# Performance work log

Measured on AMD Instinct MI355X. Metric: run time of the kernel, lower is better.

The kernel has to match this reference:

```python
import jax, jax.numpy as jnp
import numpy as np

C = 512        # feat_dim
T_LEN = 8192   # sequence length
N = 16384      # number of proposals
HID = 1024     # hidden_dim
OUT = 512      # out_dim
RATIO = 0.15   # boundary_ratio


def setup_inputs() -> dict:
    key = jax.random.key(0)
    ks = jax.random.split(key, 6)
    feat_map = jax.random.normal(ks[0], (C, T_LEN), jnp.float32)
    l = jax.random.randint(ks[1], (N,), 0, T_LEN - 64)
    width = jax.random.randint(ks[2], (N,), 8, 512)
    r = jnp.minimum(l + width, T_LEN - 1)
    W1 = jax.random.normal(ks[3], (HID, 2 * C), jnp.float32) * 0.02
    b1 = jnp.zeros((HID,), jnp.float32)
    W2 = jax.random.normal(ks[4], (OUT, HID), jnp.float32) * 0.02
    b2 = jnp.zeros((OUT,), jnp.float32)
    return {
        "feat_map": feat_map,
        "l": l.astype(jnp.int32),
        "r": r.astype(jnp.int32),
        "T": T_LEN,
        "W1": W1, "b1": b1, "W2": W2, "b2": b2,
    }


def _boundary_regions(l, r, T):
    # Mirrors: w = max(r-l, 1.0); bw = max(1, int(ratio*w)); clipped windows.
    lf = l.astype(jnp.float32)
    rf = r.astype(jnp.float32)
    w = jnp.maximum(rf - lf, 1.0)
    bw = jnp.maximum(1, (RATIO * w).astype(jnp.int32))  # int() truncation (w > 0)
    rl = jnp.round(lf).astype(jnp.int32)
    rr = jnp.round(rf).astype(jnp.int32)
    lb_s = jnp.maximum(0, rl - bw)
    lb_e = jnp.minimum(T, rl + bw)
    rb_s = jnp.maximum(0, rr - bw)
    rb_e = jnp.minimum(T, rr + bw)
    return lb_s, lb_e, rb_s, rb_e


def _pool(cs, s, e, T):
    # mean of feat[:, s:e] via inclusive prefix sums; cs: (C, T+1)
    e = jnp.maximum(s + 1, e)
    e = jnp.minimum(e, T)
    seg = cs[:, e] - cs[:, s]                      # (C, N)
    return (seg / (e - s).astype(cs.dtype)).T      # (N, C)


def reference(feat_map, l, r, T, W1, b1, W2, b2):
    # feat_map: (C, T); l, r: (N,) int proposal boundaries
    cs = jnp.concatenate(
        [jnp.zeros((feat_map.shape[0], 1), feat_map.dtype),
         jnp.cumsum(feat_map, axis=1)], axis=1)    # (C, T+1)
    lb_s, lb_e, rb_s, rb_e = _boundary_regions(l, r, T)
    e_left = _pool(cs, lb_s, lb_e, T)              # (N, C)
    e_right = _pool(cs, rb_s, rb_e, T)             # (N, C)
    e = jnp.concatenate([e_left, e_right], axis=-1)  # (N, 2C)
    h = jax.nn.relu(e @ W1.T + b1)                 # (N, HID)
    return h @ W2.T + b2                           # (N, OUT)
```

## Files before the change

### kernel.cpp

```cpp
#include <hip/hip_runtime.h>
#include <hip/hip_bf16.h>
#include <stdint.h>

#define C_DIM 512
#define T_SEQ 8192
#define N_PROP 16384
#define HID_DIM 1024
#define OUT_DIM 512
#define K2C 1024

typedef __attribute__((ext_vector_type(8))) __bf16 bf16x8;
typedef __attribute__((ext_vector_type(4))) float f32x4;

#define CFENCE() asm volatile("" ::: "memory")

__global__ __launch_bounds__(64) void cumsum_kernel(const float* __restrict__ feat,
                                                    float* __restrict__ cs_inc) {
    int c = blockIdx.x;
    const float4* in = (const float4*)(feat + (size_t)c * T_SEQ);
    float4* out = (float4*)(cs_inc + (size_t)c * T_SEQ);
    int lane = threadIdx.x;
    float carry = 0.0f;
    for (int i0 = 0; i0 < T_SEQ / 4; i0 += 64) {
        float4 v = in[i0 + lane];
        float s1 = v.x + v.y;
        float s2 = s1 + v.z;
        float s3 = s2 + v.w;
        float x = s3;
#pragma unroll
        for (int s = 1; s < 64; s <<= 1) {
            float y = __shfl_up(x, s);
            if (lane >= s) x += y;
        }
        float base = carry + (x - s3);
        float4 o;
        o.x = base + v.x; o.y = base + s1; o.z = base + s2; o.w = base + s3;
        out[i0 + lane] = o;
        carry += __shfl(x, 63);
    }
}

__global__ __launch_bounds__(256) void transpose_kernel(const float* __restrict__ cs_inc,
                                                        float* __restrict__ cs_t) {
    __shared__ float tl[32][33];
    int tx = threadIdx.x, ty = threadIdx.y;
    int x0 = blockIdx.x * 32;
    int y0 = blockIdx.y * 32;
#pragma unroll
    for (int i = 0; i < 32; i += 8) {
        int t = x0 + tx;
        int ch = y0 + ty + i;
        float v = 0.0f;
        if (t >= 1 && t <= T_SEQ) v = cs_inc[(size_t)ch * T_SEQ + (t - 1)];
        tl[ty + i][tx] = v;
    }
    __syncthreads();
#pragma unroll
    for (int i = 0; i < 32; i += 8) {
        int t = x0 + ty + i;
        int ch = y0 + tx;
        if (t <= T_SEQ) cs_t[(size_t)t * C_DIM + ch] = tl[tx][ty + i];
    }
}

__global__ __launch_bounds__(512) void pool_kernel(const float* __restrict__ cs_t,
                                                   const int* __restrict__ lptr,
                                                   const int* __restrict__ rptr,
                                                   __hip_bfloat16* __restrict__ e) {
    int n = blockIdx.x * 4 + (threadIdx.x >> 7);
    int c4 = (threadIdx.x & 127) * 4;
    int li = lptr[n], ri = rptr[n];
    float w = fmaxf((float)(ri - li), 1.0f);
    int bw = max(1, (int)(0.15f * w));
    int lb_s = max(0, li - bw);
    int lb_e = min(T_SEQ, li + bw);
    int rb_s = max(0, ri - bw);
    int rb_e = min(T_SEQ, ri + bw);
    lb_e = min(max(lb_s + 1, lb_e), T_SEQ);
    rb_e = min(max(rb_s + 1, rb_e), T_SEQ);
    float4 a = *(const float4*)(cs_t + (size_t)lb_e * C_DIM + c4);
    float4 b = *(const float4*)(cs_t + (size_t)lb_s * C_DIM + c4);
    float4 cc = *(const float4*)(cs_t + (size_t)rb_e * C_DIM + c4);
    float4 d = *(const float4*)(cs_t + (size_t)rb_s * C_DIM + c4);
    float rl = 1.0f / (float)(lb_e - lb_s);
    float rr = 1.0f / (float)(rb_e - rb_s);
    __hip_bfloat16 L0 = __float2bfloat16((a.x - b.x) * rl);
    __hip_bfloat16 L1 = __float2bfloat16((a.y - b.y) * rl);
    __hip_bfloat16 L2 = __float2bfloat16((a.z - b.z) * rl);
    __hip_bfloat16 L3 = __float2bfloat16((a.w - b.w) * rl);
    __hip_bfloat16 R0 = __float2bfloat16((cc.x - d.x) * rr);
    __hip_bfloat16 R1 = __float2bfloat16((cc.y - d.y) * rr);
    __hip_bfloat16 R2 = __float2bfloat16((cc.z - d.z) * rr);
    __hip_bfloat16 R3 = __float2bfloat16((cc.w - d.w) * rr);
    ushort4 ul, ur;
    ul.x = *(unsigned short*)&L0; ul.y = *(unsigned short*)&L1;
    ul.z = *(unsigned short*)&L2; ul.w = *(unsigned short*)&L3;
    ur.x = *(unsigned short*)&R0; ur.y = *(unsigned short*)&R1;
    ur.z = *(unsigned short*)&R2; ur.w = *(unsigned short*)&R3;
    *(ushort4*)(e + (size_t)n * K2C + c4) = ul;
    *(ushort4*)(e + (size_t)n * K2C + C_DIM + c4) = ur;
}

__global__ __launch_bounds__(256) void cvt_bf16_kernel(const float* __restrict__ W1,
                                                       const float* __restrict__ W2,
                                                       __hip_bfloat16* __restrict__ W1b,
                                                       __hip_bfloat16* __restrict__ W2b) {
    const int n1 = HID_DIM * K2C;
    int i = (blockIdx.x * 256 + threadIdx.x) * 4;
    const float* src;
    __hip_bfloat16* dst;
    int j;
    if (i < n1) { src = W1; dst = W1b; j = i; }
    else        { src = W2; dst = W2b; j = i - n1; }
    float4 v = *(const float4*)(src + j);
    __hip_bfloat16 h0 = __float2bfloat16(v.x);
    __hip_bfloat16 h1 = __float2bfloat16(v.y);
    __hip_bfloat16 h2 = __float2bfloat16(v.z);
    __hip_bfloat16 h3 = __float2bfloat16(v.w);
    ushort4 u;
    u.x = *(unsigned short*)&h0; u.y = *(unsigned short*)&h1;
    u.z = *(unsigned short*)&h2; u.w = *(unsigned short*)&h3;
    *(ushort4*)(dst + j) = u;
}

template <int BM, int BN, int WM, int WN, int RELU_BF16>
__global__ __launch_bounds__(512, 2) void gemm_pipe_kernel(const __hip_bfloat16* __restrict__ A,
                                                           const __hip_bfloat16* __restrict__ B,
                                                           const float* __restrict__ bias,
                                                           void* __restrict__ Cout,
                                                           int Nc, int K, int NBlk) {
    constexpr int BK = 64;
    constexpr int WMT = BM / WM;
    constexpr int WNT = BN / WN;
    constexpr int MR = WMT / 16;
    constexpr int NR = WNT / 16;
    constexpr int LA = BM / 64;
    constexpr int LB = BN / 64;

    __shared__ __align__(16) __hip_bfloat16 As[2][BM * BK];
    __shared__ __align__(16) __hip_bfloat16 Bs[2][BN * BK];

    const int tid = threadIdx.x;
    const int lane = tid & 63;
    const int wid = tid >> 6;
    const int wm = wid / WN;
    const int wn = wid % WN;

    const int nwg = gridDim.x;
    const int wg = (blockIdx.x & 7) * (nwg >> 3) + (blockIdx.x >> 3);
    const long m0 = (long)(wg / NBlk) * BM;
    const long n0 = (long)(wg % NBlk) * BN;

    const int srow = tid >> 3;
    const int schunk = (tid & 7) ^ (srow & 7);
    const int fr = lane & 15;
    const int g8 = (lane >> 4) * 8;

    f32x4 acc[MR][NR] = {};

    auto stageA = [&](int s, int k0) {
#pragma unroll
        for (int i = 0; i < LA; ++i)
            __builtin_amdgcn_global_load_lds(
                (const __attribute__((address_space(1))) void*)(A + (m0 + i * 64 + srow) * K + k0 + schunk * 8),
                (__attribute__((address_space(3))) void*)(&As[s][i * 4096 + tid * 8]), 16, 0, 0);
    };
    auto stageB = [&](int s, int k0) {
#pragma unroll
        for (int i = 0; i < LB; ++i)
            __builtin_amdgcn_global_load_lds(
                (const __attribute__((address_space(1))) void*)(B + (n0 + i * 64 + srow) * K + k0 + schunk * 8),
                (__attribute__((address_space(3))) void*)(&Bs[s][i * 4096 + tid * 8]), 16, 0, 0);
    };
    auto ldfrag = [&](const __hip_bfloat16* buf, int row, int kbase) -> bf16x8 {
        return *(const bf16x8*)(buf + row * 64 + ((kbase + g8) ^ ((row & 7) * 8)));
    };

    const int NT = K / BK;
    stageA(0, 0);
    stageB(0, 0);
    for (int t = 0; t < NT; ++t) {
        const int cur = t & 1;
        const __hip_bfloat16* Asc = &As[cur][0];
        const __hip_bfloat16* Bsc = &Bs[cur][0];
        if (t + 1 < NT) {
            stageA(cur ^ 1, (t + 1) * BK);
            asm volatile("s_waitcnt vmcnt(%0)" ::"n"(LA) : "memory");
        } else {
            asm volatile("s_waitcnt vmcnt(0)" ::: "memory");
        }
        __builtin_amdgcn_s_barrier();
        CFENCE();
        {
            bf16x8 af[MR], bv[NR];
#pragma unroll
            for (int m = 0; m < MR; ++m) af[m] = ldfrag(Asc, wm * WMT + m * 16 + fr, 0);
#pragma unroll
            for (int n = 0; n < NR; ++n) bv[n] = ldfrag(Bsc, wn * WNT + n * 16 + fr, 0);
            __builtin_amdgcn_s_setprio(1);
#pragma unroll
            for (int m = 0; m < MR; ++m)
#pragma unroll
                for (int n = 0; n < NR; ++n)
                    acc[m][n] = __builtin_amdgcn_mfma_f32_16x16x32_bf16(af[m], bv[n], acc[m][n], 0, 0, 0);
            __builtin_amdgcn_s_setprio(0);
        }
        if (t + 1 < NT) stageB(cur ^ 1, (t + 1) * BK);
        {
            bf16x8 af[MR], bv[NR];
#pragma unroll
            for (int m = 0; m < MR; ++m) af[m] = ldfrag(Asc, wm * WMT + m * 16 + fr, 32);
#pragma unroll
            for (int n = 0; n < NR; ++n) bv[n] = ldfrag(Bsc, wn * WNT + n * 16 + fr, 32);
            __builtin_amdgcn_s_setprio(1);
#pragma unroll
            for (int m = 0; m < MR; ++m)
#pragma unroll
                for (int n = 0; n < NR; ++n)
                    acc[m][n] = __builtin_amdgcn_mfma_f32_16x16x32_bf16(af[m], bv[n], acc[m][n], 0, 0, 0);
            __builtin_amdgcn_s_setprio(0);
        }
        CFENCE();
        __builtin_amdgcn_s_barrier();
    }

    const int rq = (lane >> 4) * 4;
#pragma unroll
    for (int m = 0; m < MR; ++m)
#pragma unroll
        for (int n = 0; n < NR; ++n) {
            long col = n0 + wn * WNT + n * 16 + fr;
            float bb = bias[col];
#pragma unroll
            for (int q = 0; q < 4; ++q) {
                long row = m0 + wm * WMT + m * 16 + rq + q;
                float v = acc[m][n][q] + bb;
                if (RELU_BF16) {
                    v = fmaxf(v, 0.0f);
                    ((__hip_bfloat16*)Cout)[row * Nc + col] = __float2bfloat16(v);
                } else {
                    ((float*)Cout)[row * Nc + col] = v;
                }
            }
        }
}

extern "C" void kernel_launch(void* const* d_in, const int* in_sizes, int n_in,
                              void* d_out, int out_size, void* d_ws, size_t ws_size,
                              hipStream_t stream) {
    const float* feat = (const float*)d_in[0];
    const int* l = (const int*)d_in[1];
    const int* r = (const int*)d_in[2];
    const float* W1 = (const float*)d_in[4];
    const float* b1 = (const float*)d_in[5];
    const float* W2 = (const float*)d_in[6];
    const float* b2 = (const float*)d_in[7];

    char* ws = (char*)d_ws;
    float* cs_t = (float*)ws;
    __hip_bfloat16* e = (__hip_bfloat16*)(ws + 16779264);
    __hip_bfloat16* h = (__hip_bfloat16*)(ws + 50333696);
    float* cs_inc = (float*)(ws + 50333696);
    __hip_bfloat16* W1b = (__hip_bfloat16*)(ws + 83888128);
    __hip_bfloat16* W2b = (__hip_bfloat16*)(ws + 85985280);

    const int ncvt = (HID_DIM * K2C + OUT_DIM * HID_DIM) / 4 / 256;
    cvt_bf16_kernel<<<dim3(ncvt), 256, 0, stream>>>(W1, W2, W1b, W2b);
    cumsum_kernel<<<dim3(C_DIM), 64, 0, stream>>>(feat, cs_inc);
    transpose_kernel<<<dim3((T_SEQ + 32) / 32, C_DIM / 32), dim3(32, 8), 0, stream>>>(cs_inc, cs_t);
    pool_kernel<<<dim3(N_PROP / 4), 512, 0, stream>>>(cs_t, l, r, e);

    gemm_pipe_kernel<256, 256, 2, 4, 1>
        <<<dim3((N_PROP / 256) * (HID_DIM / 256)), 512, 0, stream>>>(e, W1b, b1, h, HID_DIM, K2C, HID_DIM / 256);
    gemm_pipe_kernel<256, 128, 4, 2, 0>
        <<<dim3((N_PROP / 256) * (OUT_DIM / 128)), 512, 0, stream>>>(h, W2b, b2, d_out, OUT_DIM, HID_DIM, OUT_DIM / 128);
}
```

Measured before the change: 117.8 us.

## Restructure GEMM mainloop into fine-grained interleaved load/MFMA phases

Replaces the two-stage GEMM loop with a phased schedule that splits each K-tile's MFMA work into several barrier-delimited chunks. It spreads the global-to-LDS loads for the next (and next-next) tile across those chunks and prefetches part of tile u+2 into the current buffer. The goal is to hide memory latency and even out the issue of loads against matrix-core work across waves. The cost is many more barriers per iteration, and the hand-counted vmcnt waits must match the load counts exactly, which makes the schedule fragile.

New measurement: 113.1 us. 1.04x faster.

```diff
diff --git a/kernel.cpp b/kernel.cpp
--- a/kernel.cpp
+++ b/kernel.cpp
@@ -11,8 +11,6 @@
 
 typedef __attribute__((ext_vector_type(8))) __bf16 bf16x8;
 typedef __attribute__((ext_vector_type(4))) float f32x4;
-
-#define CFENCE() asm volatile("" ::: "memory")
 
 __global__ __launch_bounds__(64) void cumsum_kernel(const float* __restrict__ feat,
                                                     float* __restrict__ cs_inc) {
@@ -123,19 +121,18 @@
     *(ushort4*)(dst + j) = u;
 }
 
-template <int BM, int BN, int WM, int WN, int RELU_BF16>
-__global__ __launch_bounds__(512, 2) void gemm_pipe_kernel(const __hip_bfloat16* __restrict__ A,
-                                                           const __hip_bfloat16* __restrict__ B,
-                                                           const float* __restrict__ bias,
-                                                           void* __restrict__ Cout,
-                                                           int Nc, int K, int NBlk) {
+template <int BM, int BN, int WM, int WN, int MQ, int RELU_BF16>
+__global__ __launch_bounds__(512, 2) void gemm8p_kernel(const __hip_bfloat16* __restrict__ A,
+                                                        const __hip_bfloat16* __restrict__ B,
+                                                        const float* __restrict__ bias,
+                                                        void* __restrict__ Cout,
+                                                        int Nc, int K, int NBlk) {
     constexpr int BK = 64;
-    constexpr int WMT = BM / WM;
-    constexpr int WNT = BN / WN;
-    constexpr int MR = WMT / 16;
-    constexpr int NR = WNT / 16;
-    constexpr int LA = BM / 64;
-    constexpr int LB = BN / 64;
+    constexpr int WMT = BM / WM, WNT = BN / WN;
+    constexpr int MR = WMT / 16, NR = WNT / 16;
+    constexpr int LA = BM / 64, LB = BN / 64;
+    constexpr int U = LA + LB;
+    constexpr int CL = (MQ == 2) ? 2 : 3;
 
     __shared__ __align__(16) __hip_bfloat16 As[2][BM * BK];
     __shared__ __align__(16) __hip_bfloat16 Bs[2][BN * BK];
@@ -158,70 +155,131 @@
 
     f32x4 acc[MR][NR] = {};
 
-    auto stageA = [&](int s, int k0) {
-#pragma unroll
-        for (int i = 0; i < LA; ++i)
+    auto stage_one = [&](int s, int k0, int i) {
+        if (i < LA)
             __builtin_amdgcn_global_load_lds(
                 (const __attribute__((address_space(1))) void*)(A + (m0 + i * 64 + srow) * K + k0 + schunk * 8),
                 (__attribute__((address_space(3))) void*)(&As[s][i * 4096 + tid * 8]), 16, 0, 0);
+        else
+            __builtin_amdgcn_global_load_lds(
+                (const __attribute__((address_space(1))) void*)(B + (n0 + (i - LA) * 64 + srow) * K + k0 + schunk * 8),
+                (__attribute__((address_space(3))) void*)(&Bs[s][(i - LA) * 4096 + tid * 8]), 16, 0, 0);
     };
-    auto stageB = [&](int s, int k0) {
-#pragma unroll
-        for (int i = 0; i < LB; ++i)
-            __builtin_amdgcn_global_load_lds(
-                (const __attribute__((address_space(1))) void*)(B + (n0 + i * 64 + srow) * K + k0 + schunk * 8),
-                (__attribute__((address_space(3))) void*)(&Bs[s][i * 4096 + tid * 8]), 16, 0, 0);
+    auto ldfragA = [&](int s, int row, int kbase) -> bf16x8 {
+        return *(const bf16x8*)(&As[s][row * 64 + ((kbase + g8) ^ ((row & 7) * 8))]);
     };
-    auto ldfrag = [&](const __hip_bfloat16* buf, int row, int kbase) -> bf16x8 {
-        return *(const bf16x8*)(buf + row * 64 + ((kbase + g8) ^ ((row & 7) * 8)));
+    auto ldfragB = [&](int s, int row, int kbase) -> bf16x8 {
+        return *(const bf16x8*)(&Bs[s][row * 64 + ((kbase + g8) ^ ((row & 7) * 8))]);
     };
 
     const int NT = K / BK;
-    stageA(0, 0);
-    stageB(0, 0);
-    for (int t = 0; t < NT; ++t) {
-        const int cur = t & 1;
-        const __hip_bfloat16* Asc = &As[cur][0];
-        const __hip_bfloat16* Bsc = &Bs[cur][0];
-        if (t + 1 < NT) {
-            stageA(cur ^ 1, (t + 1) * BK);
-            asm volatile("s_waitcnt vmcnt(%0)" ::"n"(LA) : "memory");
+
+#pragma unroll
+    for (int i = 0; i < U; ++i) stage_one(0, 0, i);
+#pragma unroll
+    for (int i = 0; i < CL; ++i) stage_one(1, BK, i);
+    asm volatile("s_waitcnt vmcnt(%0)" ::"n"(CL) : "memory");
+    __builtin_amdgcn_s_barrier();
+
+    for (int u = 0; u < NT; ++u) {
+        const int cur = u & 1;
+        if constexpr (MQ == 2) {
+            bf16x8 af[MR], bv[NR];
+#pragma unroll
+            for (int m = 0; m < MR; ++m) af[m] = ldfragA(cur, wm * WMT + m * 16 + fr, 0);
+#pragma unroll
+            for (int n = 0; n < NR; ++n) bv[n] = ldfragB(cur, wn * WNT + n * 16 + fr, 0);
+            if (u + 1 < NT) { stage_one(cur ^ 1, (u + 1) * BK, 2); stage_one(cur ^ 1, (u + 1) * BK, 3); }
+            __builtin_amdgcn_s_barrier();
+            asm volatile("s_waitcnt lgkmcnt(0)" ::: "memory");
+            __builtin_amdgcn_sched_barrier(0);
+            __builtin_amdgcn_s_setprio(1);
+#pragma unroll
+            for (int m = 0; m < MR / 2; ++m)
+#pragma unroll
+                for (int n = 0; n < NR; ++n)
+                    acc[m][n] = __builtin_amdgcn_mfma_f32_16x16x32_bf16(af[m], bv[n], acc[m][n], 0, 0, 0);
+            __builtin_amdgcn_s_setprio(0);
+            __builtin_amdgcn_s_barrier();
+            if (u + 1 < NT) { stage_one(cur ^ 1, (u + 1) * BK, 4); stage_one(cur ^ 1, (u + 1) * BK, 5); }
+            __builtin_amdgcn_s_barrier();
+            __builtin_amdgcn_s_setprio(1);
+#pragma unroll
+            for (int m = MR / 2; m < MR; ++m)
+#pragma unroll
+                for (int n = 0; n < NR; ++n)
+                    acc[m][n] = __builtin_amdgcn_mfma_f32_16x16x32_bf16(af[m], bv[n], acc[m][n], 0, 0, 0);
+            __builtin_amdgcn_s_setprio(0);
+            __builtin_amdgcn_s_barrier();
+#pragma unroll
+            for (int m = 0; m < MR; ++m) af[m] = ldfragA(cur, wm * WMT + m * 16 + fr, 32);
+#pragma unroll
+            for (int n = 0; n < NR; ++n) bv[n] = ldfragB(cur, wn * WNT + n * 16 + fr, 32);
+            if (u + 1 < NT) { stage_one(cur ^ 1, (u + 1) * BK, 6); stage_one(cur ^ 1, (u + 1) * BK, 7); }
+            __builtin_amdgcn_s_barrier();
+            asm volatile("s_waitcnt lgkmcnt(0)" ::: "memory");
+            __builtin_amdgcn_sched_barrier(0);
+            __builtin_amdgcn_s_setprio(1);
+#pragma unroll
+            for (int m = 0; m < MR / 2; ++m)
+#pragma unroll
+                for (int n = 0; n < NR; ++n)
+                    acc[m][n] = __builtin_amdgcn_mfma_f32_16x16x32_bf16(af[m], bv[n], acc[m][n], 0, 0, 0);
+            __builtin_amdgcn_s_setprio(0);
+            __builtin_amdgcn_s_barrier();
+            if (u + 2 < NT) { stage_one(cur, (u + 2) * BK, 0); stage_one(cur, (u + 2) * BK, 1); }
+            if (u + 2 < NT)
+                asm volatile("s_waitcnt vmcnt(%0)" ::"n"(CL) : "memory");
+            else if (u + 1 < NT)
+                asm volatile("s_waitcnt vmcnt(0)" ::: "memory");
+            __builtin_amdgcn_s_barrier();
+            __builtin_amdgcn_s_setprio(1);
+#pragma unroll
+            for (int m = MR / 2; m < MR; ++m)
+#pragma unroll
+                for (int n = 0; n < NR; ++n)
+                    acc[m][n] = __builtin_amdgcn_mfma_f32_16x16x32_bf16(af[m], bv[n], acc[m][n], 0, 0, 0);
+            __builtin_amdgcn_s_setprio(0);
+            __builtin_amdgcn_s_barrier();
         } else {
-            asm volatile("s_waitcnt vmcnt(0)" ::: "memory");
+            bf16x8 af0[MR], af1[MR], bv0[NR], bv1[NR];
+#pragma unroll
+            for (int m = 0; m < MR; ++m) {
+                af0[m] = ldfragA(cur, wm * WMT + m * 16 + fr, 0);
+                af1[m] = ldfragA(cur, wm * WMT + m * 16 + fr, 32);
+            }
+#pragma unroll
+            for (int n = 0; n < NR; ++n) {
+                bv0[n] = ldfragB(cur, wn * WNT + n * 16 + fr, 0);
+                bv1[n] = ldfragB(cur, wn * WNT + n * 16 + fr, 32);
+            }
+            if (u + 1 < NT) { stage_one(cur ^ 1, (u + 1) * BK, 3); stage_one(cur ^ 1, (u + 1) * BK, 4); stage_one(cur ^ 1, (u + 1) * BK, 5); }
+            __builtin_amdgcn_s_barrier();
+            asm volatile("s_waitcnt lgkmcnt(0)" ::: "memory");
+            __builtin_amdgcn_sched_barrier(0);
+            __builtin_amdgcn_s_setprio(1);
+#pragma unroll
+            for (int m = 0; m < MR; ++m)
+#pragma unroll
+                for (int n = 0; n < NR; ++n)
+                    acc[m][n] = __builtin_amdgcn_mfma_f32_16x16x32_bf16(af0[m], bv0[n], acc[m][n], 0, 0, 0);
+            __builtin_amdgcn_s_setprio(0);
+            __builtin_amdgcn_s_barrier();
+            if (u + 2 < NT) { stage_one(cur, (u + 2) * BK, 0); stage_one(cur, (u + 2) * BK, 1); stage_one(cur, (u + 2) * BK, 2); }
+            if (u + 2 < NT)
+                asm volatile("s_waitcnt vmcnt(%0)" ::"n"(CL) : "memory");
+            else if (u + 1 < NT)
+                asm volatile("s_waitcnt vmcnt(0)" ::: "memory");
+            __builtin_amdgcn_s_barrier();
+            __builtin_amdgcn_s_setprio(1);
+#pragma unroll
+            for (int m = 0; m < MR; ++m)
+#pragma unroll
+                for (int n = 0; n < NR; ++n)
+                    acc[m][n] = __builtin_amdgcn_mfma_f32_16x16x32_bf16(af1[m], bv1[n], acc[m][n], 0, 0, 0);
+            __builtin_amdgcn_s_setprio(0);
+            __builtin_amdgcn_s_barrier();
         }
-        __builtin_amdgcn_s_barrier();
-        CFENCE();
-        {
-            bf16x8 af[MR], bv[NR];
-#pragma unroll
-            for (int m = 0; m < MR; ++m) af[m] = ldfrag(Asc, wm * WMT + m * 16 + fr, 0);
-#pragma unroll
-            for (int n = 0; n < NR; ++n) bv[n] = ldfrag(Bsc, wn * WNT + n * 16 + fr, 0);
-            __builtin_amdgcn_s_setprio(1);
-#pragma unroll
-            for (int m = 0; m < MR; ++m)
-#pragma unroll
-                for (int n = 0; n < NR; ++n)
-                    acc[m][n] = __builtin_amdgcn_mfma_f32_16x16x32_bf16(af[m], bv[n], acc[m][n], 0, 0, 0);
-            __builtin_amdgcn_s_setprio(0);
-        }
-        if (t + 1 < NT) stageB(cur ^ 1, (t + 1) * BK);
-        {
-            bf16x8 af[MR], bv[NR];
-#pragma unroll
-            for (int m = 0; m < MR; ++m) af[m] = ldfrag(Asc, wm * WMT + m * 16 + fr, 32);
-#pragma unroll
-            for (int n = 0; n < NR; ++n) bv[n] = ldfrag(Bsc, wn * WNT + n * 16 + fr, 32);
-            __builtin_amdgcn_s_setprio(1);
-#pragma unroll
-            for (int m = 0; m < MR; ++m)
-#pragma unroll
-                for (int n = 0; n < NR; ++n)
-                    acc[m][n] = __builtin_amdgcn_mfma_f32_16x16x32_bf16(af[m], bv[n], acc[m][n], 0, 0, 0);
-            __builtin_amdgcn_s_setprio(0);
-        }
-        CFENCE();
-        __builtin_amdgcn_s_barrier();
     }
 
     const int rq = (lane >> 4) * 4;
@@ -270,8 +328,8 @@
     transpose_kernel<<<dim3((T_SEQ + 32) / 32, C_DIM / 32), dim3(32, 8), 0, stream>>>(cs_inc, cs_t);
     pool_kernel<<<dim3(N_PROP / 4), 512, 0, stream>>>(cs_t, l, r, e);
 
-    gemm_pipe_kernel<256, 256, 2, 4, 1>
+    gemm8p_kernel<256, 256, 2, 4, 2, 1>
         <<<dim3((N_PROP / 256) * (HID_DIM / 256)), 512, 0, stream>>>(e, W1b, b1, h, HID_DIM, K2C, HID_DIM / 256);
-    gemm_pipe_kernel<256, 128, 4, 2, 0>
+    gemm8p_kernel<256, 128, 4, 2, 1, 0>
         <<<dim3((N_PROP / 256) * (OUT_DIM / 128)), 512, 0, stream>>>(h, W2b, b2, d_out, OUT_DIM, HID_DIM, OUT_DIM / 128);
 }
```

## Restructure GEMM into multi-slot prefetch pipeline with compile-time K

Applied to the files above, without the earlier changes.

Replaces the double-buffered GEMM, which split A and B staging around the two MFMA halves, with a generic NSLOT-deep ring of LDS buffers. Each slot is refilled right after it is consumed, with vmcnt waits tuned to the number of loads in flight. The first GEMM keeps two slots and the second GEMM uses three. K becomes a template parameter so the loop trip count is a compile-time constant. The aim is to hide global-to-LDS latency better, at the cost of more LDS for the 3-slot variant, which may lower occupancy, and an extra barrier per iteration.

Measured after the change: 112.9 us. 1.04x faster.

```diff
diff --git a/kernel.cpp b/kernel.cpp
--- a/kernel.cpp
+++ b/kernel.cpp
@@ -11,8 +11,6 @@
 
 typedef __attribute__((ext_vector_type(8))) __bf16 bf16x8;
 typedef __attribute__((ext_vector_type(4))) float f32x4;
-
-#define CFENCE() asm volatile("" ::: "memory")
 
 __global__ __launch_bounds__(64) void cumsum_kernel(const float* __restrict__ feat,
                                                     float* __restrict__ cs_inc) {
@@ -123,22 +121,21 @@
     *(ushort4*)(dst + j) = u;
 }
 
-template <int BM, int BN, int WM, int WN, int RELU_BF16>
-__global__ __launch_bounds__(512, 2) void gemm_pipe_kernel(const __hip_bfloat16* __restrict__ A,
-                                                           const __hip_bfloat16* __restrict__ B,
-                                                           const float* __restrict__ bias,
-                                                           void* __restrict__ Cout,
-                                                           int Nc, int K, int NBlk) {
+template <int BM, int BN, int WM, int WN, int NSLOT, int K, int RELU_BF16>
+__global__ __launch_bounds__(512, 2) void gemm_dp_kernel(const __hip_bfloat16* __restrict__ A,
+                                                         const __hip_bfloat16* __restrict__ B,
+                                                         const float* __restrict__ bias,
+                                                         void* __restrict__ Cout,
+                                                         int Nc, int NBlk) {
     constexpr int BK = 64;
-    constexpr int WMT = BM / WM;
-    constexpr int WNT = BN / WN;
-    constexpr int MR = WMT / 16;
-    constexpr int NR = WNT / 16;
-    constexpr int LA = BM / 64;
-    constexpr int LB = BN / 64;
-
-    __shared__ __align__(16) __hip_bfloat16 As[2][BM * BK];
-    __shared__ __align__(16) __hip_bfloat16 Bs[2][BN * BK];
+    constexpr int NT = K / BK;
+    constexpr int WMT = BM / WM, WNT = BN / WN;
+    constexpr int MR = WMT / 16, NR = WNT / 16;
+    constexpr int LA = BM / 64, LB = BN / 64;
+    constexpr int LPT = LA + LB;
+
+    __shared__ __align__(16) __hip_bfloat16 As[NSLOT][BM * BK];
+    __shared__ __align__(16) __hip_bfloat16 Bs[NSLOT][BN * BK];
 
     const int tid = threadIdx.x;
     const int lane = tid & 63;
@@ -158,70 +155,67 @@
 
     f32x4 acc[MR][NR] = {};
 
-    auto stageA = [&](int s, int k0) {
+    auto stage = [&](int s, int k0) {
 #pragma unroll
         for (int i = 0; i < LA; ++i)
             __builtin_amdgcn_global_load_lds(
                 (const __attribute__((address_space(1))) void*)(A + (m0 + i * 64 + srow) * K + k0 + schunk * 8),
                 (__attribute__((address_space(3))) void*)(&As[s][i * 4096 + tid * 8]), 16, 0, 0);
-    };
-    auto stageB = [&](int s, int k0) {
 #pragma unroll
         for (int i = 0; i < LB; ++i)
             __builtin_amdgcn_global_load_lds(
                 (const __attribute__((address_space(1))) void*)(B + (n0 + i * 64 + srow) * K + k0 + schunk * 8),
                 (__attribute__((address_space(3))) void*)(&Bs[s][i * 4096 + tid * 8]), 16, 0, 0);
     };
-    auto ldfrag = [&](const __hip_bfloat16* buf, int row, int kbase) -> bf16x8 {
-        return *(const bf16x8*)(buf + row * 64 + ((kbase + g8) ^ ((row & 7) * 8)));
+    auto ldA = [&](int s, int row, int kbase) -> bf16x8 {
+        return *(const bf16x8*)(&As[s][row * BK + ((kbase + g8) ^ ((row & 7) * 8))]);
     };
-
-    const int NT = K / BK;
-    stageA(0, 0);
-    stageB(0, 0);
-    for (int t = 0; t < NT; ++t) {
-        const int cur = t & 1;
-        const __hip_bfloat16* Asc = &As[cur][0];
-        const __hip_bfloat16* Bsc = &Bs[cur][0];
-        if (t + 1 < NT) {
-            stageA(cur ^ 1, (t + 1) * BK);
-            asm volatile("s_waitcnt vmcnt(%0)" ::"n"(LA) : "memory");
-        } else {
-            asm volatile("s_waitcnt vmcnt(0)" ::: "memory");
+    auto ldB = [&](int s, int row, int kbase) -> bf16x8 {
+        return *(const bf16x8*)(&Bs[s][row * BK + ((kbase + g8) ^ ((row & 7) * 8))]);
+    };
+
+#pragma unroll
+    for (int s = 0; s < NSLOT; ++s) stage(s, s * BK);
+    asm volatile("s_waitcnt vmcnt(%0)" ::"n"(LPT * (NSLOT - 1)) : "memory");
+    __builtin_amdgcn_s_barrier();
+
+    for (int u = 0; u < NT; ++u) {
+        const int cur = u % NSLOT;
+        bf16x8 af[MR], bv[NR];
+#pragma unroll
+        for (int m = 0; m < MR; ++m) af[m] = ldA(cur, wm * WMT + m * 16 + fr, 0);
+#pragma unroll
+        for (int n = 0; n < NR; ++n) bv[n] = ldB(cur, wn * WNT + n * 16 + fr, 0);
+        __builtin_amdgcn_s_setprio(1);
+#pragma unroll
+        for (int m = 0; m < MR; ++m)
+#pragma unroll
+            for (int n = 0; n < NR; ++n)
+                acc[m][n] = __builtin_amdgcn_mfma_f32_16x16x32_bf16(af[m], bv[n], acc[m][n], 0, 0, 0);
+        __builtin_amdgcn_s_setprio(0);
+#pragma unroll
+        for (int m = 0; m < MR; ++m) af[m] = ldA(cur, wm * WMT + m * 16 + fr, 32);
+#pragma unroll
+        for (int n = 0; n < NR; ++n) bv[n] = ldB(cur, wn * WNT + n * 16 + fr, 32);
+        __builtin_amdgcn_s_setprio(1);
+#pragma unroll
+        for (int m = 0; m < MR; ++m)
+#pragma unroll
+            for (int n = 0; n < NR; ++n)
+                acc[m][n] = __builtin_amdgcn_mfma_f32_16x16x32_bf16(af[m], bv[n], acc[m][n], 0, 0, 0);
+        __builtin_amdgcn_s_setprio(0);
+
+        __builtin_amdgcn_s_barrier();
+        if (u + NSLOT < NT) stage(cur, (u + NSLOT) * BK);
+        if (u + 1 < NT) {
+            if (u + NSLOT < NT)
+                asm volatile("s_waitcnt vmcnt(%0)" ::"n"(LPT * (NSLOT - 1)) : "memory");
+            else if (NSLOT == 3 && u + 2 < NT)
+                asm volatile("s_waitcnt vmcnt(%0)" ::"n"(LPT) : "memory");
+            else
+                asm volatile("s_waitcnt vmcnt(0)" ::: "memory");
+            __builtin_amdgcn_s_barrier();
         }
-        __builtin_amdgcn_s_barrier();
-        CFENCE();
-        {
-            bf16x8 af[MR], bv[NR];
-#pragma unroll
-            for (int m = 0; m < MR; ++m) af[m] = ldfrag(Asc, wm * WMT + m * 16 + fr, 0);
-#pragma unroll
-            for (int n = 0; n < NR; ++n) bv[n] = ldfrag(Bsc, wn * WNT + n * 16 + fr, 0);
-            __builtin_amdgcn_s_setprio(1);
-#pragma unroll
-            for (int m = 0; m < MR; ++m)
-#pragma unroll
-                for (int n = 0; n < NR; ++n)
-                    acc[m][n] = __builtin_amdgcn_mfma_f32_16x16x32_bf16(af[m], bv[n], acc[m][n], 0, 0, 0);
-            __builtin_amdgcn_s_setprio(0);
-        }
-        if (t + 1 < NT) stageB(cur ^ 1, (t + 1) * BK);
-        {
-            bf16x8 af[MR], bv[NR];
-#pragma unroll
-            for (int m = 0; m < MR; ++m) af[m] = ldfrag(Asc, wm * WMT + m * 16 + fr, 32);
-#pragma unroll
-            for (int n = 0; n < NR; ++n) bv[n] = ldfrag(Bsc, wn * WNT + n * 16 + fr, 32);
-            __builtin_amdgcn_s_setprio(1);
-#pragma unroll
-            for (int m = 0; m < MR; ++m)
-#pragma unroll
-                for (int n = 0; n < NR; ++n)
-                    acc[m][n] = __builtin_amdgcn_mfma_f32_16x16x32_bf16(af[m], bv[n], acc[m][n], 0, 0, 0);
-            __builtin_amdgcn_s_setprio(0);
-        }
-        CFENCE();
-        __builtin_amdgcn_s_barrier();
     }
 
     const int rq = (lane >> 4) * 4;
@@ -270,8 +264,8 @@
     transpose_kernel<<<dim3((T_SEQ + 32) / 32, C_DIM / 32), dim3(32, 8), 0, stream>>>(cs_inc, cs_t);
     pool_kernel<<<dim3(N_PROP / 4), 512, 0, stream>>>(cs_t, l, r, e);
 
-    gemm_pipe_kernel<256, 256, 2, 4, 1>
-        <<<dim3((N_PROP / 256) * (HID_DIM / 256)), 512, 0, stream>>>(e, W1b, b1, h, HID_DIM, K2C, HID_DIM / 256);
-    gemm_pipe_kernel<256, 128, 4, 2, 0>
-        <<<dim3((N_PROP / 256) * (OUT_DIM / 128)), 512, 0, stream>>>(h, W2b, b2, d_out, OUT_DIM, HID_DIM, OUT_DIM / 128);
-}
+    gemm_dp_kernel<256, 256, 2, 4, 2, K2C, 1>
+        <<<dim3((N_PROP / 256) * (HID_DIM / 256)), 512, 0, stream>>>(e, W1b, b1, h, HID_DIM, HID_DIM / 256);
+    gemm_dp_kernel<256, 128, 4, 2, 3, HID_DIM, 0>
+        <<<dim3((N_PROP / 256) * (OUT_DIM / 128)), 512, 0, stream>>>(h, W2b, b2, d_out, OUT_DIM, OUT_DIM / 128);
+}
```
